# Performance work log

Hardware: AMD Instinct MI355X
Metric: run time of the kernel (lower is better)

## Reference

```python
import jax, jax.numpy as jnp
import numpy as np

D = 512      # hidden_size
H = 8        # num_heads
DK = D // H  # head dim
B, T = 8, 1024
EPS = 1e-5


def setup_inputs() -> dict:
    key = jax.random.key(0)
    ks = jax.random.split(key, 12)
    s = 0.02
    return {
        "x": jax.random.normal(ks[0], (B, T, D), jnp.float32),
        "xlens": jax.random.randint(ks[1], (B,), 1, T + 1, jnp.int32),
        "pos_emb": jax.random.normal(ks[2], (1, 2 * T - 1, D), jnp.float32),
        "ln_gamma": jnp.ones((D,), jnp.float32),
        "ln_beta": jnp.zeros((D,), jnp.float32),
        "Wq": jax.random.normal(ks[3], (D, D), jnp.float32) * s,
        "bq": jnp.zeros((D,), jnp.float32),
        "Wk": jax.random.normal(ks[4], (D, D), jnp.float32) * s,
        "bk": jnp.zeros((D,), jnp.float32),
        "Wv": jax.random.normal(ks[5], (D, D), jnp.float32) * s,
        "bv": jnp.zeros((D,), jnp.float32),
        "Wpos": jax.random.normal(ks[6], (D, D), jnp.float32) * s,  # no bias
        "pos_bias_u": jax.random.normal(ks[7], (H, DK), jnp.float32) * s,
        "pos_bias_v": jax.random.normal(ks[8], (H, DK), jnp.float32) * s,
        "Wo": jax.random.normal(ks[9], (D, D), jnp.float32) * s,
        "bo": jnp.zeros((D,), jnp.float32),
    }


def _rel_shift(x):
    # Transformer-XL shift trick: (B, H, T, 2T-1) -> (B, H, T, T)
    b, h, t, n = x.shape
    x = jnp.pad(x, ((0, 0), (0, 0), (0, 0), (1, 0)))       # (b,h,t,2t)
    x = x.reshape(b, h, n + 1, t)[:, :, 1:, :].reshape(b, h, t, n)
    return x[..., :t]


def reference(x, xlens, pos_emb, ln_gamma, ln_beta, Wq, bq, Wk, bk, Wv, bv,
              Wpos, pos_bias_u, pos_bias_v, Wo, bo):
    b, t, d = x.shape
    # LayerNorm
    mu = jnp.mean(x, axis=-1, keepdims=True)
    var = jnp.mean(jnp.square(x - mu), axis=-1, keepdims=True)
    xn = (x - mu) * jax.lax.rsqrt(var + EPS) * ln_gamma + ln_beta

    # key padding mask: True where index >= len (padded)
    pad_mask = jnp.arange(t)[None, :] >= xlens[:, None]      # (B, T)

    q = (xn @ Wq + bq).reshape(b, t, H, DK)                  # (B,T,H,DK)
    k = (xn @ Wk + bk).reshape(b, t, H, DK)
    v = (xn @ Wv + bv).reshape(b, t, H, DK)
    p = (pos_emb @ Wpos).reshape(-1, H, DK)                  # (2T-1,H,DK)

    q_u = q + pos_bias_u                                     # (B,T,H,DK)
    q_v = q + pos_bias_v

    # content score + positional score (Transformer-XL)
    matrix_ac = jnp.einsum('bthd,bshd->bhts', q_u, k)        # (B,H,T,T)
    matrix_bd = jnp.einsum('bthd,nhd->bhtn', q_v, p)         # (B,H,T,2T-1)
    matrix_bd = _rel_shift(matrix_bd)                        # (B,H,T,T)

    scores = (matrix_ac + matrix_bd) / jnp.sqrt(jnp.float32(DK))
    scores = jnp.where(pad_mask[:, None, None, :], jnp.float32(-1e9), scores)
    attn = jax.nn.softmax(scores, axis=-1)
    attn = jnp.where(pad_mask[:, None, None, :], 0.0, attn)
    # dropout prob applied only in training; eval mode -> identity

    out = jnp.einsum('bhts,bshd->bthd', attn, v).reshape(b, t, d)
    out = out @ Wo + bo
    return out, xlens
```

## Files before the change

kernel.cpp:

```cpp
#include <hip/hip_runtime.h>
#include <stdint.h>


typedef __attribute__((ext_vector_type(8))) short s8v;
typedef __attribute__((ext_vector_type(4))) short s4v;
typedef __attribute__((ext_vector_type(4))) float f4v;
typedef unsigned short u16;

#define MFMA(a, b, c) __builtin_amdgcn_mfma_f32_16x16x32_bf16((a), (b), (c), 0, 0, 0)

__device__ __forceinline__ float bf2f(u16 u) {
    union { unsigned i; float f; } w; w.i = ((unsigned)u) << 16; return w.f;
}
__device__ __forceinline__ u16 f2bf(float f) {
    union { float f; unsigned i; } w; w.f = f;
    return (u16)((w.i + 0x7FFFu + ((w.i >> 16) & 1u)) >> 16);
}
__device__ __forceinline__ u16 f2bt(float f) {
    union { float f; unsigned i; } w; w.f = f;
    return (u16)(w.i >> 16);
}
__device__ __forceinline__ void gld16(const void* g, void* l) {
    __builtin_amdgcn_global_load_lds(
        (const __attribute__((address_space(1))) unsigned int*)g,
        (__attribute__((address_space(3))) unsigned int*)l, 16, 0, 0);
}

__global__ __launch_bounds__(256) void prep_k(
    const float* __restrict__ Wq, const float* __restrict__ Wk, const float* __restrict__ Wv,
    const float* __restrict__ Wpos, const float* __restrict__ Wo,
    const float* __restrict__ pos_emb, const int* __restrict__ xlens,
    const float* __restrict__ x, const float* __restrict__ gamma,
    const float* __restrict__ beta,
    u16* __restrict__ wt, u16* __restrict__ pe, float* __restrict__ tail,
    u16* __restrict__ xn)
{
    int bid = blockIdx.x, tid = threadIdx.x;
    if (bid < 1280) {
        __shared__ float lt[32][33];
        int mat = bid >> 8, tile = bid & 255;
        int kt = (tile >> 4) << 5, nt = (tile & 15) << 5;
        const float* W = mat == 0 ? Wq : mat == 1 ? Wk : mat == 2 ? Wv : mat == 3 ? Wpos : Wo;
        int ty = tid >> 3, tx = tid & 7;
        float4 vv = *(const float4*)&W[(kt + ty) * 512 + nt + tx * 4];
        lt[ty][tx * 4 + 0] = vv.x; lt[ty][tx * 4 + 1] = vv.y;
        lt[ty][tx * 4 + 2] = vv.z; lt[ty][tx * 4 + 3] = vv.w;
        __syncthreads();
        int nl = tid >> 3, k4 = (tid & 7) * 4;
        union { s4v v; u16 u[4]; } ob;
        #pragma unroll
        for (int e = 0; e < 4; ++e) ob.u[e] = f2bf(lt[k4 + e][nl]);
        *(s4v*)&wt[mat * 262144 + (nt + nl) * 512 + kt + k4] = ob.v;
    } else if (bid < 2304) {
        int i = (bid - 1280) * 1024 + tid * 4;
        union { s4v v; u16 u[4]; } ob;
        if (i < 2047 * 512) {
            float4 vv = *(const float4*)&pos_emb[i];
            ob.u[0] = f2bf(vv.x); ob.u[1] = f2bf(vv.y);
            ob.u[2] = f2bf(vv.z); ob.u[3] = f2bf(vv.w);
        } else {
            ob.u[0] = ob.u[1] = ob.u[2] = ob.u[3] = 0;
        }
        *(s4v*)&pe[i] = ob.v;
    } else if (bid == 2304) {
        if (tid < 8) tail[tid] = (float)xlens[tid];
    } else {
        int tok = (bid - 2305) * 4 + (tid >> 6);
        int l = tid & 63;
        const float* xr = x + (size_t)tok * 512 + l * 8;
        float v[8];
        {
            float4 a = *(const float4*)xr; float4 b = *(const float4*)(xr + 4);
            v[0] = a.x; v[1] = a.y; v[2] = a.z; v[3] = a.w;
            v[4] = b.x; v[5] = b.y; v[6] = b.z; v[7] = b.w;
        }
        float s = 0.f, q = 0.f;
        #pragma unroll
        for (int e = 0; e < 8; ++e) { s += v[e]; q += v[e] * v[e]; }
        #pragma unroll
        for (int off = 1; off < 64; off <<= 1) { s += __shfl_xor(s, off); q += __shfl_xor(q, off); }
        float mean = s * (1.f / 512.f);
        float var = q * (1.f / 512.f) - mean * mean;
        float inv = rsqrtf(var + 1e-5f);
        union { s8v v; u16 u[8]; } ob;
        #pragma unroll
        for (int e = 0; e < 8; ++e)
            ob.u[e] = f2bf((v[e] - mean) * inv * gamma[l * 8 + e] + beta[l * 8 + e]);
        *(s8v*)&xn[(size_t)tok * 512 + l * 8] = ob.v;
    }
}

__global__ __launch_bounds__(256, 2) void gemm_k(
    const u16* __restrict__ A, const u16* __restrict__ Ap, const u16* __restrict__ wt,
    const float* __restrict__ bq, const float* __restrict__ bk, const float* __restrict__ bv,
    int mode, u16* __restrict__ qo, u16* __restrict__ ko, u16* __restrict__ vtg,
    u16* __restrict__ pb, float* __restrict__ of)
{
    __shared__ u16 Al[2][128 * 64];
    __shared__ u16 Bl[2][128 * 64];
    int tid = threadIdx.x, l = tid & 63, wid = tid >> 6;
    int wr = wid >> 1, wc = wid & 1, r = l & 15, g = l >> 4;
    int m0, nb, mat;
    const u16 *Ag, *Wg;
    if (mode == 0) {
        if (blockIdx.y < 12) {
            m0 = blockIdx.x << 7; int n0 = blockIdx.y << 7;
            mat = n0 >> 9; nb = n0 & 511; Ag = A; Wg = wt + mat * 262144;
        } else {
            mat = 3; m0 = (blockIdx.x & 15) << 7; nb = (blockIdx.x >> 4) << 7;
            Ag = Ap; Wg = wt + 3 * 262144;
        }
    } else {
        mat = 4; m0 = blockIdx.x << 7; nb = blockIdx.y << 7; Ag = A; Wg = wt + 4 * 262144;
    }

    int rw8 = l >> 3;
    int csw = ((l & 7) ^ rw8) << 3;
    int off0 = ((g ^ (r & 7)) << 3);
    int off1 = (((4 + g) ^ (r & 7)) << 3);

    f4v zero = {0.f, 0.f, 0.f, 0.f};
    f4v acc[4][4];
    #pragma unroll
    for (int i = 0; i < 4; ++i)
        #pragma unroll
        for (int j = 0; j < 4; ++j) acc[i][j] = zero;

    #pragma unroll
    for (int it = 0; it < 4; ++it) {
        int rowb = wid * 32 + it * 8;
        gld16(&Ag[(size_t)(m0 + rowb + rw8) * 512 + csw], &Al[0][rowb * 64]);
        gld16(&Wg[(size_t)(nb + rowb + rw8) * 512 + csw], &Bl[0][rowb * 64]);
    }
    __syncthreads();

    for (int t = 0; t < 8; ++t) {
        int cur = t & 1;
        if (t < 7) {
            int k1 = (t + 1) << 6;
            #pragma unroll
            for (int it = 0; it < 4; ++it) {
                int rowb = wid * 32 + it * 8;
                gld16(&Ag[(size_t)(m0 + rowb + rw8) * 512 + k1 + csw], &Al[cur ^ 1][rowb * 64]);
                gld16(&Wg[(size_t)(nb + rowb + rw8) * 512 + k1 + csw], &Bl[cur ^ 1][rowb * 64]);
            }
        }
        s8v af[4][2], bfv[4][2];
        #pragma unroll
        for (int i = 0; i < 4; ++i) {
            int row = (wr * 64 + i * 16 + r) * 64;
            af[i][0] = *(const s8v*)&Al[cur][row + off0];
            af[i][1] = *(const s8v*)&Al[cur][row + off1];
        }
        #pragma unroll
        for (int j = 0; j < 4; ++j) {
            int row = (wc * 64 + j * 16 + r) * 64;
            bfv[j][0] = *(const s8v*)&Bl[cur][row + off0];
            bfv[j][1] = *(const s8v*)&Bl[cur][row + off1];
        }
        __builtin_amdgcn_s_setprio(1);
        #pragma unroll
        for (int i = 0; i < 4; ++i)
            #pragma unroll
            for (int j = 0; j < 4; ++j) {
                acc[i][j] = MFMA(af[i][0], bfv[j][0], acc[i][j]);
                acc[i][j] = MFMA(af[i][1], bfv[j][1], acc[i][j]);
            }
        __builtin_amdgcn_s_setprio(0);
        __syncthreads();
    }

    #pragma unroll
    for (int i = 0; i < 4; ++i)
        #pragma unroll
        for (int j = 0; j < 4; ++j) {
            int ncol = nb + wc * 64 + j * 16 + r;
            int mbase = m0 + wr * 64 + i * 16 + g * 4;
            if (mode == 2) {
                float bb = bq[ncol];
                #pragma unroll
                for (int jj = 0; jj < 4; ++jj)
                    of[(size_t)(mbase + jj) * 512 + ncol] = acc[i][j][jj] + bb;
            } else if (mat == 3) {
                int hh = ncol >> 6, dk = ncol & 63;
                #pragma unroll
                for (int jj = 0; jj < 4; ++jj) {
                    int m = mbase + jj;
                    if (m < 2047) pb[(hh * 2047 + m) * 64 + dk] = f2bf(acc[i][j][jj]);
                }
            } else if (mat == 2) {
                float bb = bv[ncol];
                int hh = ncol >> 6, dk = ncol & 63;
                int bbx = mbase >> 10, t = mbase & 1023;
                union { s4v v; u16 u[4]; } pk;
                #pragma unroll
                for (int jj = 0; jj < 4; ++jj) pk.u[jj] = f2bf(acc[i][j][jj] + bb);
                *(s4v*)&vtg[((size_t)(bbx * 8 + hh) * 64 + dk) * 1024 + t] = pk.v;
            } else {
                float bb = (mat == 0 ? bq : bk)[ncol];
                u16* dst = (mat == 0) ? qo : ko;
                int hh = ncol >> 6, dk = ncol & 63;
                #pragma unroll
                for (int jj = 0; jj < 4; ++jj) {
                    int m = mbase + jj;
                    int bbx = m >> 10, t = m & 1023;
                    dst[((size_t)(bbx * 8 + hh) * 1024 + t) * 64 + dk] = f2bf(acc[i][j][jj] + bb);
                }
            }
        }
}

__global__ __launch_bounds__(512, 4) void attn_k(
    const u16* __restrict__ q, const u16* __restrict__ k, const u16* __restrict__ vtg,
    const u16* __restrict__ p, const float* __restrict__ pbu, const float* __restrict__ pbv,
    const int* __restrict__ xlens, u16* __restrict__ ao)
{
    __shared__ u16 Ks[2][64 * 64];
    __shared__ u16 Vt[64 * 64];
    __shared__ u16 Ps[256 * 64];
    __shared__ u16 Tb[8][16 * 72];

    int tid = threadIdx.x, l = tid & 63, wid = tid >> 6;
    int r = l & 15, g = l >> 4, kq = g << 3;

    int l8[8];
    #pragma unroll
    for (int e = 0; e < 8; ++e) l8[e] = xlens[e];
    int ell = blockIdx.x;
    int slot = ell >> 8, m = ell & 255;
    int kr = m >> 6; if (slot) kr = 7 - kr;
    int b = 0;
    #pragma unroll
    for (int e = 0; e < 8; ++e) {
        int rk = 0;
        #pragma unroll
        for (int j = 0; j < 8; ++j)
            rk += (l8[j] > l8[e]) || (l8[j] == l8[e] && j < e);
        if (rk == kr) b = e;
    }
    int rem = m & 63;
    int h = rem >> 3;
    int t0 = (rem & 7) << 7;
    int tw = t0 + wid * 16;
    int xlen = l8[b];

    const u16* qh = q + (size_t)(b * 8 + h) * 65536;
    const u16* kh = k + (size_t)(b * 8 + h) * 65536;
    const u16* vh = vtg + (size_t)(b * 8 + h) * 65536;
    const u16* ph = p + (size_t)h * 2047 * 64;

    int rw8 = l >> 3;
    int csw = ((l & 7) ^ rw8) << 3;
    int off0 = ((g ^ (r & 7)) << 3);
    int off1 = (((4 + g) ^ (r & 7)) << 3);

    const float SCALE = 0.18033688f;

    s8v qu[2], qv[2];
    #pragma unroll
    for (int ks = 0; ks < 2; ++ks) {
        union { s8v v; u16 u[8]; } src, du, dv;
        src.v = *(const s8v*)&qh[(tw + r) * 64 + ks * 32 + kq];
        float4 u0 = *(const float4*)&pbu[h * 64 + ks * 32 + kq];
        float4 u1 = *(const float4*)&pbu[h * 64 + ks * 32 + kq + 4];
        float4 v0 = *(const float4*)&pbv[h * 64 + ks * 32 + kq];
        float4 v1 = *(const float4*)&pbv[h * 64 + ks * 32 + kq + 4];
        float ub[8] = {u0.x, u0.y, u0.z, u0.w, u1.x, u1.y, u1.z, u1.w};
        float vb_[8] = {v0.x, v0.y, v0.z, v0.w, v1.x, v1.y, v1.z, v1.w};
        #pragma unroll
        for (int e = 0; e < 8; ++e) {
            float qf = bf2f(src.u[e]);
            du.u[e] = f2bf((qf + ub[e]) * SCALE);
            dv.u[e] = f2bf((qf + vb_[e]) * SCALE);
        }
        qu[ks] = du.v; qv[ks] = dv.v;
    }

    int B0 = 896 - t0;
    int nst = (xlen + 63) >> 6;

    {
        int rowb = wid * 8;
        gld16(&kh[(rowb + rw8) * 64 + csw], &Ks[0][rowb * 64]);
        gld16(&vh[(rowb + rw8) * 1024 + csw], &Vt[rowb * 64]);
    }
    #pragma unroll
    for (int it = 0; it < 3; ++it) {
        int row = wid * 24 + it * 8;
        int slot2 = (B0 + row) & 255;
        gld16(&ph[(size_t)(B0 + row + rw8) * 64 + csw], &Ps[slot2 * 64]);
    }
    __syncthreads();

    float lst[4] = {0.f, 0.f, 0.f, 0.f};
    f4v zero = {0.f, 0.f, 0.f, 0.f};
    f4v o[4] = {zero, zero, zero, zero};
    u16* tb = &Tb[wid][0];

    for (int i = 0; i < nst; ++i) {
        int cur = i & 1, s0 = i << 6;
        if (i > 0) {
            int rowb = wid * 8;
            gld16(&vh[(rowb + rw8) * 1024 + s0 + csw], &Vt[rowb * 64]);
        }
        if (i + 1 < nst) {
            int s1 = s0 + 64;
            int rowb = wid * 8;
            gld16(&kh[(s1 + rowb + rw8) * 64 + csw], &Ks[cur ^ 1][rowb * 64]);
            int chunk = B0 + 192 + s0 + wid * 8;
            int slot2 = chunk & 255;
            int gp = chunk + rw8; gp = gp > 2046 ? 2046 : gp;
            gld16(&ph[(size_t)gp * 64 + csw], &Ps[slot2 * 64]);
        }
        const u16* KB = &Ks[cur][0];
        f4v st4[4];
        __builtin_amdgcn_s_setprio(1);
        #pragma unroll
        for (int nf = 0; nf < 4; ++nf) {
            int row = (nf * 16 + r) * 64;
            s8v k0 = *(const s8v*)&KB[row + off0];
            s8v k1 = *(const s8v*)&KB[row + off1];
            st4[nf] = MFMA(qu[1], k1, MFMA(qu[0], k0, zero));
        }
        int pstart = 1008 + s0 - tw;
        f4v bst[5];
        #pragma unroll
        for (int pf = 0; pf < 5; ++pf) {
            int slot2 = (pstart + pf * 16 + r) & 255;
            const u16* rowp = &Ps[slot2 * 64];
            f4v a = MFMA(qv[0], *(const s8v*)&rowp[off0], zero);
            bst[pf] = MFMA(qv[1], *(const s8v*)&rowp[off1], a);
        }
        __builtin_amdgcn_s_setprio(0);
        bool full = (s0 + 64 <= xlen);
        float pr[4][4];
        #pragma unroll
        for (int j = 0; j < 4; ++j) {
            int tl = g * 4 + j;
            int d = r + 15 - tl;
            int al = ((g << 4) | (d & 15)) << 2;
            unsigned w0 = (unsigned)f2bt(bst[0][j]) | ((unsigned)f2bt(bst[1][j]) << 16);
            unsigned w1 = (unsigned)f2bt(bst[2][j]) | ((unsigned)f2bt(bst[3][j]) << 16);
            unsigned w2 = (unsigned)f2bt(bst[4][j]);
            unsigned p0 = (unsigned)__builtin_amdgcn_ds_bpermute(al, (int)w0);
            unsigned p1 = (unsigned)__builtin_amdgcn_ds_bpermute(al, (int)w1);
            unsigned p2 = (unsigned)__builtin_amdgcn_ds_bpermute(al, (int)w2);
            bool lo = d < 16;
            float bds[4];
            bds[0] = bf2f((u16)(lo ? (p0 & 0xffffu) : (p0 >> 16)));
            bds[1] = bf2f((u16)(lo ? (p0 >> 16) : (p1 & 0xffffu)));
            bds[2] = bf2f((u16)(lo ? (p1 & 0xffffu) : (p1 >> 16)));
            bds[3] = bf2f((u16)(lo ? (p1 >> 16) : (p2 & 0xffffu)));
            #pragma unroll
            for (int nf = 0; nf < 4; ++nf) {
                float e = exp2f(st4[nf][j] + bds[nf]);
                if (!full) e = (s0 + nf * 16 + r >= xlen) ? 0.f : e;
                pr[nf][j] = e;
            }
        }
        #pragma unroll
        for (int j = 0; j < 4; ++j)
            lst[j] += (pr[0][j] + pr[1][j]) + (pr[2][j] + pr[3][j]);
        #pragma unroll
        for (int nf = 0; nf < 4; ++nf)
            #pragma unroll
            for (int j = 0; j < 4; ++j)
                tb[(g * 4 + j) * 72 + nf * 16 + r] = f2bt(pr[nf][j]);
        asm volatile("s_waitcnt lgkmcnt(0)" ::: "memory");
        __builtin_amdgcn_sched_barrier(0);
        s8v pa0 = *(const s8v*)&tb[r * 72 + kq];
        s8v pa1 = *(const s8v*)&tb[r * 72 + 32 + kq];
        if (i > 0) {
            if (i + 1 < nst) asm volatile("s_waitcnt vmcnt(2)" ::: "memory");
            else             asm volatile("s_waitcnt vmcnt(0)" ::: "memory");
        }
        __builtin_amdgcn_s_setprio(1);
        #pragma unroll
        for (int i2 = 0; i2 < 4; ++i2) {
            int vrow = (i2 * 16 + r) * 64;
            o[i2] = MFMA(pa0, *(const s8v*)&Vt[vrow + off0], o[i2]);
            o[i2] = MFMA(pa1, *(const s8v*)&Vt[vrow + off1], o[i2]);
        }
        __builtin_amdgcn_s_setprio(0);
        __syncthreads();
    }
    #pragma unroll
    for (int j = 0; j < 4; ++j) {
        float rs = lst[j];
        rs += __shfl_xor(rs, 1); rs += __shfl_xor(rs, 2);
        rs += __shfl_xor(rs, 4); rs += __shfl_xor(rs, 8);
        float inv = 1.f / rs;
        int t = tw + g * 4 + j;
        #pragma unroll
        for (int i2 = 0; i2 < 4; ++i2)
            ao[((size_t)(b * 1024 + t)) * 512 + h * 64 + i2 * 16 + r] = f2bf(o[i2][j] * inv);
    }
}

extern "C" void kernel_launch(void* const* d_in, const int* in_sizes, int n_in,
                              void* d_out, int out_size, void* d_ws, size_t ws_size,
                              hipStream_t stream)
{
    (void)in_sizes; (void)n_in; (void)out_size; (void)ws_size;
    const float* x     = (const float*)d_in[0];
    const int*   xlens = (const int*)d_in[1];
    const float* pos_e = (const float*)d_in[2];
    const float* gam   = (const float*)d_in[3];
    const float* bet   = (const float*)d_in[4];
    const float* Wq    = (const float*)d_in[5];
    const float* bq    = (const float*)d_in[6];
    const float* Wk    = (const float*)d_in[7];
    const float* bk    = (const float*)d_in[8];
    const float* Wv    = (const float*)d_in[9];
    const float* bv    = (const float*)d_in[10];
    const float* Wpos  = (const float*)d_in[11];
    const float* pbu   = (const float*)d_in[12];
    const float* pbv   = (const float*)d_in[13];
    const float* Wo    = (const float*)d_in[14];
    const float* bo    = (const float*)d_in[15];
    float* out = (float*)d_out;

    char* ws = (char*)d_ws;
    u16* xn  = (u16*)(ws);
    u16* qb  = (u16*)(ws + 8388608);
    u16* kb  = (u16*)(ws + 16777216);
    u16* vtg = (u16*)(ws + 25165824);
    u16* pbf = (u16*)(ws + 33554432);
    u16* pe  = (u16*)(ws + 35651584);
    u16* wt  = (u16*)(ws + 37748736);

    prep_k<<<4353, 256, 0, stream>>>(Wq, Wk, Wv, Wpos, Wo, pos_e, xlens,
                                     x, gam, bet, wt, pe,
                                     out + (size_t)8192 * 512, xn);
    gemm_k<<<dim3(64, 13), 256, 0, stream>>>(xn, pe, wt, bq, bk, bv, 0,
                                             qb, kb, vtg, pbf, nullptr);
    attn_k<<<dim3(512), 512, 0, stream>>>(qb, kb, vtg, pbf, pbu, pbv, xlens, xn);
    gemm_k<<<dim3(64, 4), 256, 0, stream>>>(xn, nullptr, wt, bo, nullptr, nullptr, 2,
                                            nullptr, nullptr, nullptr, nullptr, out);
}
```

Before: 98.76 us.

## Split long-sequence attention over key halves and merge partial sums

Batches with xlen > 512 now have their key range split into two halves, each handled by its own block, and the grid doubles to 1024 blocks. Heavy blocks write unnormalised bf16 partial outputs and row sums, and a new merge kernel adds the halves and normalises them. The old xlens-ranked block ordering, which balanced load across blocks, is replaced by this split-K scheme. This adds an extra launch, workspace traffic for the partials, and extra bf16 rounding of the partial outputs. Merging without a max is valid only because the softmax carries no running max (plain exp2).

```diff
diff --git a/kernel.cpp b/kernel.cpp
--- a/kernel.cpp
+++ b/kernel.cpp
@@ -213,7 +213,8 @@
 __global__ __launch_bounds__(512, 4) void attn_k(
     const u16* __restrict__ q, const u16* __restrict__ k, const u16* __restrict__ vtg,
     const u16* __restrict__ p, const float* __restrict__ pbu, const float* __restrict__ pbv,
-    const int* __restrict__ xlens, u16* __restrict__ ao)
+    const int* __restrict__ xlens, u16* __restrict__ ao,
+    u16* __restrict__ o_part, float* __restrict__ l_part)
 {
     __shared__ u16 Ks[2][64 * 64];
     __shared__ u16 Vt[64 * 64];
@@ -223,26 +224,19 @@
     int tid = threadIdx.x, l = tid & 63, wid = tid >> 6;
     int r = l & 15, g = l >> 4, kq = g << 3;
 
-    int l8[8];
-    #pragma unroll
-    for (int e = 0; e < 8; ++e) l8[e] = xlens[e];
-    int ell = blockIdx.x;
-    int slot = ell >> 8, m = ell & 255;
-    int kr = m >> 6; if (slot) kr = 7 - kr;
-    int b = 0;
-    #pragma unroll
-    for (int e = 0; e < 8; ++e) {
-        int rk = 0;
-        #pragma unroll
-        for (int j = 0; j < 8; ++j)
-            rk += (l8[j] > l8[e]) || (l8[j] == l8[e] && j < e);
-        if (rk == kr) b = e;
-    }
+    int half = blockIdx.x >> 9;
+    int m = blockIdx.x & 511;
+    int b = m >> 6;
     int rem = m & 63;
     int h = rem >> 3;
     int t0 = (rem & 7) << 7;
     int tw = t0 + wid * 16;
-    int xlen = l8[b];
+    int xlen = xlens[b];
+    int nst_total = (xlen + 63) >> 6;
+    bool heavy = xlen > 512;
+    if (half && !heavy) return;
+    int n_this = half ? (nst_total - 8) : (nst_total < 8 ? nst_total : 8);
+    int s_base = half << 9;
 
     const u16* qh = q + (size_t)(b * 8 + h) * 65536;
     const u16* kh = k + (size_t)(b * 8 + h) * 65536;
@@ -276,19 +270,19 @@
         qu[ks] = du.v; qv[ks] = dv.v;
     }
 
-    int B0 = 896 - t0;
-    int nst = (xlen + 63) >> 6;
+    int B0 = 896 - t0 + s_base;
 
     {
         int rowb = wid * 8;
-        gld16(&kh[(rowb + rw8) * 64 + csw], &Ks[0][rowb * 64]);
-        gld16(&vh[(rowb + rw8) * 1024 + csw], &Vt[rowb * 64]);
+        gld16(&kh[(s_base + rowb + rw8) * 64 + csw], &Ks[0][rowb * 64]);
+        gld16(&vh[(rowb + rw8) * 1024 + s_base + csw], &Vt[rowb * 64]);
     }
     #pragma unroll
     for (int it = 0; it < 3; ++it) {
         int row = wid * 24 + it * 8;
+        int gp = B0 + row + rw8; gp = gp > 2046 ? 2046 : gp;
         int slot2 = (B0 + row) & 255;
-        gld16(&ph[(size_t)(B0 + row + rw8) * 64 + csw], &Ps[slot2 * 64]);
+        gld16(&ph[(size_t)gp * 64 + csw], &Ps[slot2 * 64]);
     }
     __syncthreads();
 
@@ -297,17 +291,17 @@
     f4v o[4] = {zero, zero, zero, zero};
     u16* tb = &Tb[wid][0];
 
-    for (int i = 0; i < nst; ++i) {
-        int cur = i & 1, s0 = i << 6;
+    for (int i = 0; i < n_this; ++i) {
+        int cur = i & 1, srel = i << 6, s0 = s_base + srel;
         if (i > 0) {
             int rowb = wid * 8;
             gld16(&vh[(rowb + rw8) * 1024 + s0 + csw], &Vt[rowb * 64]);
         }
-        if (i + 1 < nst) {
+        if (i + 1 < n_this) {
             int s1 = s0 + 64;
             int rowb = wid * 8;
             gld16(&kh[(s1 + rowb + rw8) * 64 + csw], &Ks[cur ^ 1][rowb * 64]);
-            int chunk = B0 + 192 + s0 + wid * 8;
+            int chunk = B0 + 192 + srel + wid * 8;
             int slot2 = chunk & 255;
             int gp = chunk + rw8; gp = gp > 2046 ? 2046 : gp;
             gld16(&ph[(size_t)gp * 64 + csw], &Ps[slot2 * 64]);
@@ -371,8 +365,8 @@
         s8v pa0 = *(const s8v*)&tb[r * 72 + kq];
         s8v pa1 = *(const s8v*)&tb[r * 72 + 32 + kq];
         if (i > 0) {
-            if (i + 1 < nst) asm volatile("s_waitcnt vmcnt(2)" ::: "memory");
-            else             asm volatile("s_waitcnt vmcnt(0)" ::: "memory");
+            if (i + 1 < n_this) asm volatile("s_waitcnt vmcnt(2)" ::: "memory");
+            else                asm volatile("s_waitcnt vmcnt(0)" ::: "memory");
         }
         __builtin_amdgcn_s_setprio(1);
         #pragma unroll
@@ -384,16 +378,57 @@
         __builtin_amdgcn_s_setprio(0);
         __syncthreads();
     }
-    #pragma unroll
-    for (int j = 0; j < 4; ++j) {
-        float rs = lst[j];
-        rs += __shfl_xor(rs, 1); rs += __shfl_xor(rs, 2);
-        rs += __shfl_xor(rs, 4); rs += __shfl_xor(rs, 8);
-        float inv = 1.f / rs;
-        int t = tw + g * 4 + j;
-        #pragma unroll
-        for (int i2 = 0; i2 < 4; ++i2)
-            ao[((size_t)(b * 1024 + t)) * 512 + h * 64 + i2 * 16 + r] = f2bf(o[i2][j] * inv);
+    if (!heavy) {
+        #pragma unroll
+        for (int j = 0; j < 4; ++j) {
+            float rs = lst[j];
+            rs += __shfl_xor(rs, 1); rs += __shfl_xor(rs, 2);
+            rs += __shfl_xor(rs, 4); rs += __shfl_xor(rs, 8);
+            float inv = 1.f / rs;
+            int t = tw + g * 4 + j;
+            #pragma unroll
+            for (int i2 = 0; i2 < 4; ++i2)
+                ao[((size_t)(b * 1024 + t)) * 512 + h * 64 + i2 * 16 + r] = f2bf(o[i2][j] * inv);
+        }
+    } else {
+        u16* op = o_part + (size_t)half * 4194304;
+        float* lp = l_part + half * 65536;
+        #pragma unroll
+        for (int j = 0; j < 4; ++j) {
+            float rs = lst[j];
+            rs += __shfl_xor(rs, 1); rs += __shfl_xor(rs, 2);
+            rs += __shfl_xor(rs, 4); rs += __shfl_xor(rs, 8);
+            int t = tw + g * 4 + j;
+            if (r == 0) lp[(b * 8 + h) * 1024 + t] = rs;
+            #pragma unroll
+            for (int i2 = 0; i2 < 4; ++i2)
+                op[((size_t)(b * 1024 + t)) * 512 + h * 64 + i2 * 16 + r] = f2bf(o[i2][j]);
+        }
+    }
+}
+
+__global__ __launch_bounds__(256) void merge_k(
+    const u16* __restrict__ o_part, const float* __restrict__ l_part,
+    const int* __restrict__ xlens, u16* __restrict__ ao)
+{
+    int b = blockIdx.x >> 3, tc = blockIdx.x & 7;
+    if (xlens[b] <= 512) return;
+    int tid = threadIdx.x;
+    for (int v = tid; v < 8192; v += 256) {
+        int elem = v << 3;
+        int t = tc * 128 + (elem >> 9);
+        int col = elem & 511;
+        int h = col >> 6;
+        float lsum = l_part[(b * 8 + h) * 1024 + t] + l_part[65536 + (b * 8 + h) * 1024 + t];
+        float inv = 1.f / lsum;
+        size_t idx = ((size_t)(b * 1024 + t)) * 512 + col;
+        union { s8v v; u16 u[8]; } a0, a1, ob;
+        a0.v = *(const s8v*)&o_part[idx];
+        a1.v = *(const s8v*)&o_part[4194304 + idx];
+        #pragma unroll
+        for (int e = 0; e < 8; ++e)
+            ob.u[e] = f2bf((bf2f(a0.u[e]) + bf2f(a1.u[e])) * inv);
+        *(s8v*)&ao[idx] = ob.v;
     }
 }
 
@@ -421,20 +456,24 @@
     float* out = (float*)d_out;
 
     char* ws = (char*)d_ws;
-    u16* xn  = (u16*)(ws);
-    u16* qb  = (u16*)(ws + 8388608);
-    u16* kb  = (u16*)(ws + 16777216);
-    u16* vtg = (u16*)(ws + 25165824);
-    u16* pbf = (u16*)(ws + 33554432);
-    u16* pe  = (u16*)(ws + 35651584);
-    u16* wt  = (u16*)(ws + 37748736);
+    u16* xn   = (u16*)(ws);
+    u16* qb   = (u16*)(ws + 8388608);
+    u16* kb   = (u16*)(ws + 16777216);
+    u16* vtg  = (u16*)(ws + 25165824);
+    u16* pbf  = (u16*)(ws + 33554432);
+    u16* pe   = (u16*)(ws + 35651584);
+    u16* wt   = (u16*)(ws + 37748736);
+    u16* opart = (u16*)(ws + 40370176);
+    float* lpart = (float*)(ws + 57147392);
 
     prep_k<<<4353, 256, 0, stream>>>(Wq, Wk, Wv, Wpos, Wo, pos_e, xlens,
                                      x, gam, bet, wt, pe,
                                      out + (size_t)8192 * 512, xn);
     gemm_k<<<dim3(64, 13), 256, 0, stream>>>(xn, pe, wt, bq, bk, bv, 0,
                                              qb, kb, vtg, pbf, nullptr);
-    attn_k<<<dim3(512), 512, 0, stream>>>(qb, kb, vtg, pbf, pbu, pbv, xlens, xn);
+    attn_k<<<dim3(1024), 512, 0, stream>>>(qb, kb, vtg, pbf, pbu, pbv, xlens, xn,
+                                           opart, lpart);
+    merge_k<<<dim3(64), 256, 0, stream>>>(opart, lpart, xlens, xn);
     gemm_k<<<dim3(64, 4), 256, 0, stream>>>(xn, nullptr, wt, bo, nullptr, nullptr, 2,
                                             nullptr, nullptr, nullptr, nullptr, out);
 }
```

New measurement: 117.0 us. 18.5% more time.
